# Performance work log

Hardware: AMD Instinct MI355X
Metric: run time of the kernel (lower is better)

Reference implementation:

```python
import jax, jax.numpy as jnp
import numpy as np

# dataset / mesh constants (from ds_props)
NX_PATCH, NY_PATCH = 10, 6       # Nx_patch * Ny_patch == 60 (hardcoded N_patch)
PX = 16                          # patch_size == out_patch_size
NPX, NPY = NX_PATCH * PX, NY_PATCH * PX
N_NODES = NPX * NPY              # 15360
HID = 128


def make_edge_idx(n, m):
    """Bidirectional 4-neighbor grid edges; n rows, m cols; node idx = j*n + i."""
    jj, ii = np.meshgrid(np.arange(m), np.arange(n - 1), indexing='ij')
    a = (jj * n + ii).ravel()
    e_v = np.concatenate([np.stack([a, a + 1]), np.stack([a + 1, a])], axis=1)
    ii2, jj2 = np.meshgrid(np.arange(n), np.arange(m - 1), indexing='ij')
    b = (jj2 * n + ii2).ravel()
    e_h = np.concatenate([np.stack([b, b + n]), np.stack([b + n, b])], axis=1)
    return np.concatenate([e_v, e_h], axis=1).astype(np.int32)  # [2, E]


def setup_inputs() -> dict:
    key = jax.random.key(0)
    ks = jax.random.split(key, 6)
    bs, seq_len, in_dim = 4, 32, 1024
    s = 0.02
    return {
        'patch_vectors': jax.random.normal(ks[0], (bs, seq_len * 60, in_dim), jnp.float32),
        'W1': jax.random.normal(ks[1], (in_dim, 512), jnp.float32) * s,
        'b1': jnp.zeros((512,), jnp.float32),
        'W2': jax.random.normal(ks[2], (512, HID), jnp.float32) * s,
        'b2': jnp.zeros((HID,), jnp.float32),
        'Wg': jax.random.normal(ks[3], (HID + 4, 3), jnp.float32) * s,
        'bg': jnp.zeros((3,), jnp.float32),
        'edge_index': jnp.asarray(make_edge_idx(NPY, NPX)),  # make_edge_idx(Ny_mesh, Nx_mesh)
    }


def _coord_feats():
    # patch index per pixel: (Npx, Npy, 2), raw integer patch coords (as in source)
    xg, yg = jnp.meshgrid(jnp.arange(NX_PATCH), jnp.arange(NY_PATCH), indexing='ij')
    pidx = jnp.stack([xg, yg], axis=-1).astype(jnp.float32)          # (Nx_patch, Ny_patch, 2)
    pidx = jnp.repeat(jnp.repeat(pidx, PX, axis=0), PX, axis=1)       # (Npx, Npy, 2)
    # pixel index within patch, normalized by global max (px-1), tiled over patches
    xp, yp = jnp.meshgrid(jnp.arange(PX), jnp.arange(PX), indexing='ij')
    pix = jnp.stack([xp, yp], axis=-1).astype(jnp.float32) / (PX - 1)
    pix = jnp.tile(pix, (NX_PATCH, NY_PATCH, 1))                      # (Npx, Npy, 2)
    return pidx, pix


def reference(patch_vectors, W1, b1, W2, b2, Wg, bg, edge_index):
    bs, tot_patchs, _ = patch_vectors.shape
    seq_len = tot_patchs // 60
    # input MLP: Linear -> softplus -> Linear
    h = jax.nn.softplus(patch_vectors @ W1 + b1) @ W2 + b2            # (bs, tot, 128)
    h = h.reshape(bs, seq_len, NX_PATCH, NY_PATCH, HID)
    # patch_to_px: repeat_interleave upsample to pixel mesh
    h = jnp.repeat(jnp.repeat(h, PX, axis=2), PX, axis=3)             # (bs, seq, Npx, Npy, 128)
    pidx, pix = _coord_feats()
    pidx = jnp.broadcast_to(pidx, (bs, seq_len, NPX, NPY, 2))
    pix = jnp.broadcast_to(pix, (bs, seq_len, NPX, NPY, 2))
    feat = jnp.concatenate([h, pidx, pix], axis=-1)                   # (..., 132)
    feat = feat.reshape(bs * seq_len, N_NODES, HID + 4)               # (B, N, 132)
    # GCNConv with self-loops: D^{-1/2} (A+I) D^{-1/2} X W + b
    src, dst = edge_index[0], edge_index[1]
    deg = 1.0 + jax.ops.segment_sum(jnp.ones(src.shape, jnp.float32), dst, num_segments=N_NODES)
    dinv = jax.lax.rsqrt(deg)
    norm = dinv[src] * dinv[dst]                                      # (E,)
    xw = feat @ Wg                                                    # (B, N, 3)
    agg = jax.vmap(lambda m: jax.ops.segment_sum(m, dst, num_segments=N_NODES))(
        xw[:, src, :] * norm[None, :, None])                          # scatter-add over edges
    out = agg + xw * (1.0 / deg)[None, :, None] + bg                  # self-loop term + bias
    return out.reshape(-1, NPX, NPY, 3)
```

## Files before the change

kernel.cpp:

```cpp
#include <hip/hip_runtime.h>
#include <math.h>

typedef __bf16 bf16_t;
typedef __bf16 bf16x8 __attribute__((ext_vector_type(8)));
typedef float f32x4 __attribute__((ext_vector_type(4)));

#define M_ROWS 7680
#define N1 512
#define K1 1024
#define NPX 160
#define NPY 96
#define BDIM 128
#define NPATCH 60
#define NPIX (BDIM*NPX*NPY)

#define OFF_WGEFF   0
#define OFF_BIASEFF 1536
#define OFF_CF      2048
#define OFF_HWPART  71168
#define OFF_W1T     255488

#define BM 64
#define BN 64
#define BK 64
#define LDT 72

__global__ __launch_bounds__(256) void prep_kernel(
    const float* __restrict__ W1, const float* __restrict__ W2,
    const float* __restrict__ b2, const float* __restrict__ Wg,
    const float* __restrict__ bg, float* __restrict__ ws)
{
    const int t = threadIdx.x;
    if (blockIdx.x < 128) {
        __shared__ bf16_t tile[64][72];
        const int k0 = (blockIdx.x & 15) * 64;
        const int n0 = (blockIdx.x >> 4) * 64;
        bf16_t* W1T = (bf16_t*)(ws + OFF_W1T);
#pragma unroll
        for (int i = 0; i < 4; ++i) {
            int idx = t + i * 256;
            int r = idx >> 4, ch = idx & 15;
            float4 v = *(const float4*)(W1 + (size_t)(k0 + r) * N1 + n0 + ch * 4);
            bf16_t* dst = &tile[r][ch * 4];
            dst[0] = (bf16_t)v.x; dst[1] = (bf16_t)v.y;
            dst[2] = (bf16_t)v.z; dst[3] = (bf16_t)v.w;
        }
        __syncthreads();
#pragma unroll
        for (int i = 0; i < 2; ++i) {
            int idx = t + i * 256;
            int nr = idx >> 3, kc = idx & 7;
            bf16x8 o;
#pragma unroll
            for (int j = 0; j < 8; ++j) o[j] = tile[kc * 8 + j][nr];
            *(bf16x8*)(W1T + (size_t)(n0 + nr) * K1 + k0 + kc * 8) = o;
        }
    } else if (blockIdx.x == 128) {
#pragma unroll
        for (int rep = 0; rep < 2; ++rep) {
            int j = t + rep * 256;
            float a0 = 0.f, a1 = 0.f, a2 = 0.f;
            for (int k = 0; k < 128; ++k) {
                float w = W2[j * 128 + k];
                a0 = fmaf(w, Wg[k * 3 + 0], a0);
                a1 = fmaf(w, Wg[k * 3 + 1], a1);
                a2 = fmaf(w, Wg[k * 3 + 2], a2);
            }
            ws[OFF_WGEFF + j * 3 + 0] = a0;
            ws[OFF_WGEFF + j * 3 + 1] = a1;
            ws[OFF_WGEFF + j * 3 + 2] = a2;
        }
        if (t < 3) {
            float s = 0.f;
            for (int k = 0; k < 128; ++k) s = fmaf(b2[k], Wg[k * 3 + t], s);
            ws[OFF_BIASEFF + t] = s;
        }
    } else {
        int e = (blockIdx.x - 129) * 256 + t;
        int c = e % 3;
        int p = e / 3;
        int x = p / NPY, y = p % NPY;
        float wpx = Wg[128 * 3 + c], wpy = Wg[129 * 3 + c];
        float wqx = Wg[130 * 3 + c], wqy = Wg[131 * 3 + c];
        auto aff = [&](int xx, int yy) -> float {
            return (float)(xx >> 4) * wpx + (float)(yy >> 4) * wpy
                 + (float)(xx & 15) * (1.f / 15.f) * wqx
                 + (float)(yy & 15) * (1.f / 15.f) * wqy;
        };
        auto deg = [&](int xx, int yy) -> float {
            return 1.f + (xx > 0) + (xx < NPX - 1) + (yy > 0) + (yy < NPY - 1);
        };
        float degc = deg(x, y);
        float s = 0.f;
        if (x > 0)       s += rsqrtf(deg(x - 1, y)) * aff(x - 1, y);
        if (x < NPX - 1) s += rsqrtf(deg(x + 1, y)) * aff(x + 1, y);
        if (y > 0)       s += rsqrtf(deg(x, y - 1)) * aff(x, y - 1);
        if (y < NPY - 1) s += rsqrtf(deg(x, y + 1)) * aff(x, y + 1);
        ws[OFF_CF + e] = rsqrtf(degc) * s + aff(x, y) / degc + bg[c];
    }
}

static __device__ inline bf16x8 cvt8(float4 a, float4 b) {
    bf16x8 v;
    v[0] = (bf16_t)a.x; v[1] = (bf16_t)a.y; v[2] = (bf16_t)a.z; v[3] = (bf16_t)a.w;
    v[4] = (bf16_t)b.x; v[5] = (bf16_t)b.y; v[6] = (bf16_t)b.z; v[7] = (bf16_t)b.w;
    return v;
}

__global__ __launch_bounds__(512, 8) void gemm_mfma_kernel(
    const float* __restrict__ A,
    const float* __restrict__ b1,
    const float* __restrict__ ws,
    float* __restrict__ hw_part)
{
    __shared__ __align__(16) char smem[36864];
    bf16_t* sA = (bf16_t*)smem;
    bf16_t* sB = sA + 2 * BM * LDT;
    float* red = (float*)smem;
    const bf16_t* W1T = (const bf16_t*)(ws + OFF_W1T);

    const int bid = blockIdx.x;
    const int xcd = bid & 7;
    const int local = bid >> 3;
    const int nblk = local & 7;
    const int mblk = xcd * 15 + (local >> 3);
    const int m0 = mblk * BM;
    const int n0 = nblk * BN;

    const int t = threadIdx.x;
    const int lane = t & 63;
    const int wv = t >> 6;
    const int wr = wv & 1;
    const int wcn = wv >> 1;
    const int l15 = lane & 15, hi = lane >> 4;

    const int srow = t >> 3;
    const int oct = (t & 7) << 3;
    const float*  aptr = A   + (size_t)(m0 + srow) * K1 + oct;
    const bf16_t* bptr = W1T + (size_t)(n0 + srow) * K1 + oct;
    const int swoff = srow * LDT + oct;

    f32x4 acc[2];
    acc[0] = (f32x4)0.f; acc[1] = (f32x4)0.f;

    {
        float4 fa0 = *(const float4*)(aptr + 0);
        float4 fa1 = *(const float4*)(aptr + 4);
        uint4  ub0 = *(const uint4*)(bptr);
        *(bf16x8*)(sA + swoff) = cvt8(fa0, fa1);
        *(uint4*)(sB + swoff)  = ub0;
    }
    __syncthreads();

    int cur = 0;
    for (int ks = 0; ks < K1 / BK; ++ks) {
        float4 fa0, fa1; uint4 ub0;
        const bool pf = (ks < K1 / BK - 1);
        if (pf) {
            const float*  ap = aptr + (ks + 1) * BK;
            const bf16_t* bp = bptr + (ks + 1) * BK;
            fa0 = *(const float4*)(ap + 0);
            fa1 = *(const float4*)(ap + 4);
            ub0 = *(const uint4*)(bp);
        }
        const bf16_t* cA = sA + cur * (BM * LDT);
        const bf16_t* cB = sB + cur * (BM * LDT);
        bf16x8 af[2][2], bfr[2];
#pragma unroll
        for (int kk = 0; kk < 2; ++kk) {
#pragma unroll
            for (int mi = 0; mi < 2; ++mi)
                af[mi][kk] = *(const bf16x8*)(cA + (wr * 32 + mi * 16 + l15) * LDT + kk * 32 + hi * 8);
            bfr[kk] = *(const bf16x8*)(cB + (wcn * 16 + l15) * LDT + kk * 32 + hi * 8);
        }
#pragma unroll
        for (int kk = 0; kk < 2; ++kk)
#pragma unroll
            for (int mi = 0; mi < 2; ++mi)
                acc[mi] = __builtin_amdgcn_mfma_f32_16x16x32_bf16(
                    af[mi][kk], bfr[kk], acc[mi], 0, 0, 0);
        if (pf) {
            bf16_t* nA = sA + (cur ^ 1) * (BM * LDT);
            bf16_t* nB = sB + (cur ^ 1) * (BM * LDT);
            *(bf16x8*)(nA + swoff) = cvt8(fa0, fa1);
            *(uint4*)(nB + swoff)  = ub0;
        }
        __syncthreads();
        cur ^= 1;
    }

    const int n = n0 + wcn * 16 + l15;
    const float bb = b1[n];
    const float wg0 = ws[OFF_WGEFF + n * 3 + 0];
    const float wg1 = ws[OFF_WGEFF + n * 3 + 1];
    const float wg2 = ws[OFF_WGEFF + n * 3 + 2];
    const int jslot = (wcn & 1) * 16 + l15;

    float p[2][4][3];
#pragma unroll
    for (int mi = 0; mi < 2; ++mi)
#pragma unroll
        for (int r = 0; r < 4; ++r) {
            float z = acc[mi][r] + bb;
            float sp = fmaxf(z, 0.f) + __logf(1.f + __expf(-fabsf(z)));
            p[mi][r][0] = sp * wg0;
            p[mi][r][1] = sp * wg1;
            p[mi][r][2] = sp * wg2;
        }
    __syncthreads();
    if (wcn < 2) {
#pragma unroll
        for (int mi = 0; mi < 2; ++mi)
#pragma unroll
            for (int r = 0; r < 4; ++r) {
                int ml = wr * 32 + mi * 16 + hi * 4 + r;
                float* dst = red + (ml * 32 + jslot) * 3;
                dst[0] = p[mi][r][0]; dst[1] = p[mi][r][1]; dst[2] = p[mi][r][2];
            }
    }
    __syncthreads();
    if (wcn >= 2) {
#pragma unroll
        for (int mi = 0; mi < 2; ++mi)
#pragma unroll
            for (int r = 0; r < 4; ++r) {
                int ml = wr * 32 + mi * 16 + hi * 4 + r;
                float* dst = red + (ml * 32 + jslot) * 3;
                dst[0] += p[mi][r][0]; dst[1] += p[mi][r][1]; dst[2] += p[mi][r][2];
            }
    }
    __syncthreads();
    if (t < 192) {
        int m = t / 3, c = t - m * 3;
        float s = 0.f;
#pragma unroll
        for (int j = 0; j < 32; ++j) s += red[(m * 32 + j) * 3 + c];
        hw_part[((size_t)nblk * M_ROWS + m0 + m) * 3 + c] = s;
    }
}

__global__ __launch_bounds__(384) void stencil_kernel(
    const float* __restrict__ ws, float* __restrict__ out)
{
    __shared__ float hwl[3][6][3];
    const int blk = blockIdx.x;
    const int b = blk / 10;
    const int px0 = blk % 10;
    const int x0 = px0 * 16;
    const int t = threadIdx.x;

    if (t < 54) {
        int j = t / 3, c = t - (t / 3) * 3;
        int dxi = j / 6, py = j % 6;
        int px = px0 - 1 + dxi;
        float v = 0.f;
        if (px >= 0 && px < 10) {
            int m = b * NPATCH + px * 6 + py;
            v = ws[OFF_BIASEFF + c];
#pragma unroll
            for (int s = 0; s < 8; ++s)
                v += ws[OFF_HWPART + ((size_t)s * M_ROWS + m) * 3 + c];
        }
        hwl[dxi][py][c] = v;
    }
    __syncthreads();

    const int xr = t / 24;
    const int y0 = (t - xr * 24) * 4;
    const int x = x0 + xr;
    const float* cf = ws + OFF_CF;

    auto deg = [&](int xx, int yy) -> float {
        return 1.f + (xx > 0) + (xx < NPX - 1) + (yy > 0) + (yy < NPY - 1);
    };
    auto hwp = [&](int xx, int yy) -> const float* {
        return &hwl[(xx >> 4) - (px0 - 1)][yy >> 4][0];
    };

    float res[4][3];
#pragma unroll
    for (int i = 0; i < 4; ++i) {
        int y = y0 + i;
        float degc = deg(x, y);
        float dinvc = rsqrtf(degc);
        float s0 = 0.f, s1 = 0.f, s2 = 0.f;
        auto tap = [&](int xx, int yy) {
            float dn = rsqrtf(deg(xx, yy));
            const float* h = hwp(xx, yy);
            s0 = fmaf(dn, h[0], s0);
            s1 = fmaf(dn, h[1], s1);
            s2 = fmaf(dn, h[2], s2);
        };
        if (x > 0)       tap(x - 1, y);
        if (x < NPX - 1) tap(x + 1, y);
        if (y > 0)       tap(x, y - 1);
        if (y < NPY - 1) tap(x, y + 1);
        const float* hs = hwp(x, y);
        const float* c = cf + (x * NPY + y) * 3;
        float inv_deg = 1.f / degc;
        res[i][0] = c[0] + fmaf(dinvc, s0, hs[0] * inv_deg);
        res[i][1] = c[1] + fmaf(dinvc, s1, hs[1] * inv_deg);
        res[i][2] = c[2] + fmaf(dinvc, s2, hs[2] * inv_deg);
    }
    float4 v0 = {res[0][0], res[0][1], res[0][2], res[1][0]};
    float4 v1 = {res[1][1], res[1][2], res[2][0], res[2][1]};
    float4 v2 = {res[2][2], res[3][0], res[3][1], res[3][2]};
    size_t p0 = ((size_t)b * NPX + x) * NPY + y0;
    float* o = out + p0 * 3;
    *(float4*)(o + 0) = v0;
    *(float4*)(o + 4) = v1;
    *(float4*)(o + 8) = v2;
}

extern "C" void kernel_launch(void* const* d_in, const int* in_sizes, int n_in,
                              void* d_out, int out_size, void* d_ws, size_t ws_size,
                              hipStream_t stream) {
    const float* pv = (const float*)d_in[0];
    const float* W1 = (const float*)d_in[1];
    const float* b1 = (const float*)d_in[2];
    const float* W2 = (const float*)d_in[3];
    const float* b2 = (const float*)d_in[4];
    const float* Wg = (const float*)d_in[5];
    const float* bg = (const float*)d_in[6];

    float* ws = (float*)d_ws;
    float* out = (float*)d_out;

    hipLaunchKernelGGL(prep_kernel, dim3(309), dim3(256), 0, stream,
                       W1, W2, b2, Wg, bg, ws);
    hipLaunchKernelGGL(gemm_mfma_kernel, dim3(960), dim3(512), 0, stream,
                       pv, b1, ws, ws + OFF_HWPART);
    hipLaunchKernelGGL(stencil_kernel, dim3(1280), dim3(384), 0, stream,
                       ws, out);
}
```

Measured before the change: 55.17 us.

## Pre-convert activations to bf16 and stream GEMM tiles via global_load_lds

When the workspace is large enough, the prep kernel gains 960 extra blocks that convert the fp32 activation matrix to bf16 in workspace. A new 256-thread GEMM kernel then loads swizzled bf16 A and W1T tiles directly into LDS with global_load_lds, double-buffered, so the fp32 loads and in-register conversion leave the GEMM loop. The cost is an extra full write and re-read of a 15 MB bf16 copy of A plus an added dependency between prep and GEMM. If the workspace is too small, the old path is kept.

```diff
diff --git a/kernel.cpp b/kernel.cpp
--- a/kernel.cpp
+++ b/kernel.cpp
@@ -4,6 +4,7 @@
 typedef __bf16 bf16_t;
 typedef __bf16 bf16x8 __attribute__((ext_vector_type(8)));
 typedef float f32x4 __attribute__((ext_vector_type(4)));
+typedef unsigned int u32;
 
 #define M_ROWS 7680
 #define N1 512
@@ -19,16 +20,32 @@
 #define OFF_CF      2048
 #define OFF_HWPART  71168
 #define OFF_W1T     255488
+#define OFF_ABF     517632
+#define WS_NEED_BYTES ((size_t)OFF_ABF * 4 + (size_t)M_ROWS * K1 * 2)
 
 #define BM 64
 #define BN 64
 #define BK 64
 #define LDT 72
 
+static __device__ __forceinline__ void gll16(const void* g, void* l) {
+    __builtin_amdgcn_global_load_lds(
+        (const __attribute__((address_space(1))) u32*)g,
+        (__attribute__((address_space(3))) u32*)l, 16, 0, 0);
+}
+
+static __device__ inline bf16x8 cvt8(float4 a, float4 b) {
+    bf16x8 v;
+    v[0] = (bf16_t)a.x; v[1] = (bf16_t)a.y; v[2] = (bf16_t)a.z; v[3] = (bf16_t)a.w;
+    v[4] = (bf16_t)b.x; v[5] = (bf16_t)b.y; v[6] = (bf16_t)b.z; v[7] = (bf16_t)b.w;
+    return v;
+}
+
 __global__ __launch_bounds__(256) void prep_kernel(
-    const float* __restrict__ W1, const float* __restrict__ W2,
-    const float* __restrict__ b2, const float* __restrict__ Wg,
-    const float* __restrict__ bg, float* __restrict__ ws)
+    const float* __restrict__ A, const float* __restrict__ W1,
+    const float* __restrict__ W2, const float* __restrict__ b2,
+    const float* __restrict__ Wg, const float* __restrict__ bg,
+    float* __restrict__ ws)
 {
     const int t = threadIdx.x;
     if (blockIdx.x < 128) {
@@ -75,7 +92,7 @@
             for (int k = 0; k < 128; ++k) s = fmaf(b2[k], Wg[k * 3 + t], s);
             ws[OFF_BIASEFF + t] = s;
         }
-    } else {
+    } else if (blockIdx.x < 309) {
         int e = (blockIdx.x - 129) * 256 + t;
         int c = e % 3;
         int p = e / 3;
@@ -97,21 +114,151 @@
         if (y > 0)       s += rsqrtf(deg(x, y - 1)) * aff(x, y - 1);
         if (y < NPY - 1) s += rsqrtf(deg(x, y + 1)) * aff(x, y + 1);
         ws[OFF_CF + e] = rsqrtf(degc) * s + aff(x, y) / degc + bg[c];
-    }
-}
-
-static __device__ inline bf16x8 cvt8(float4 a, float4 b) {
-    bf16x8 v;
-    v[0] = (bf16_t)a.x; v[1] = (bf16_t)a.y; v[2] = (bf16_t)a.z; v[3] = (bf16_t)a.w;
-    v[4] = (bf16_t)b.x; v[5] = (bf16_t)b.y; v[6] = (bf16_t)b.z; v[7] = (bf16_t)b.w;
-    return v;
-}
-
-__global__ __launch_bounds__(512, 8) void gemm_mfma_kernel(
-    const float* __restrict__ A,
+    } else {
+        bf16_t* Abf = (bf16_t*)(ws + OFF_ABF);
+        const int m0 = (blockIdx.x - 309) * 8;
+#pragma unroll
+        for (int j = 0; j < 4; ++j) {
+            int c = t + j * 256;
+            int row = c >> 7;
+            int col8 = c & 127;
+            const float* src = A + (size_t)(m0 + row) * K1 + col8 * 8;
+            float4 v0 = *(const float4*)(src);
+            float4 v1 = *(const float4*)(src + 4);
+            *(bf16x8*)(Abf + (size_t)(m0 + row) * K1 + col8 * 8) = cvt8(v0, v1);
+        }
+    }
+}
+
+__global__ __launch_bounds__(256) void gemm_gll_kernel(
     const float* __restrict__ b1,
     const float* __restrict__ ws,
     float* __restrict__ hw_part)
+{
+    __shared__ __align__(16) char smem[32768];
+    bf16_t* sA = (bf16_t*)smem;
+    bf16_t* sB = sA + 2 * 64 * 64;
+    float* red = (float*)smem;
+    const bf16_t* W1T = (const bf16_t*)(ws + OFF_W1T);
+    const bf16_t* Abf = (const bf16_t*)(ws + OFF_ABF);
+
+    const int bid = blockIdx.x;
+    const int xcd = bid & 7;
+    const int local = bid >> 3;
+    const int nblk = local & 7;
+    const int mblk = xcd * 15 + (local >> 3);
+    const int m0 = mblk * BM;
+    const int n0 = nblk * BN;
+
+    const int t = threadIdx.x;
+    const int lane = t & 63;
+    const int wv = t >> 6;
+    const int wr = wv >> 1, wc = wv & 1;
+    const int l15 = lane & 15, hi = lane >> 4;
+    const int x7 = l15 & 7;
+
+    const int rbase0 = 8 * (2 * wv + 0) + (lane >> 3);
+    const int c16src = (lane & 7) ^ (lane >> 3);
+    const bf16_t* aSrc0 = Abf + (size_t)(m0 + rbase0) * K1 + c16src * 8;
+    const bf16_t* aSrc1 = aSrc0 + (size_t)8 * K1;
+    const bf16_t* bSrc0 = W1T + (size_t)(n0 + rbase0) * K1 + c16src * 8;
+    const bf16_t* bSrc1 = bSrc0 + (size_t)8 * K1;
+    const int ldsOffA0 = (2 * wv + 0) * 512;
+    const int ldsOffA1 = (2 * wv + 1) * 512;
+
+    int aoff[2][2], boff[2][2];
+#pragma unroll
+    for (int mi = 0; mi < 2; ++mi)
+#pragma unroll
+        for (int kk = 0; kk < 2; ++kk) {
+            aoff[mi][kk] = (wr * 32 + mi * 16 + l15) * 64 + ((kk * 4 + hi) ^ x7) * 8;
+            boff[mi][kk] = (wc * 32 + mi * 16 + l15) * 64 + ((kk * 4 + hi) ^ x7) * 8;
+        }
+
+    f32x4 acc[2][2];
+#pragma unroll
+    for (int i = 0; i < 2; ++i)
+#pragma unroll
+        for (int j = 0; j < 2; ++j) acc[i][j] = (f32x4)0.f;
+
+    gll16(aSrc0, sA + ldsOffA0);
+    gll16(aSrc1, sA + ldsOffA1);
+    gll16(bSrc0, sB + ldsOffA0);
+    gll16(bSrc1, sB + ldsOffA1);
+    __syncthreads();
+
+    int cur = 0;
+    for (int ks = 0; ks < K1 / BK; ++ks) {
+        if (ks < K1 / BK - 1) {
+            const int koff = (ks + 1) * BK;
+            const int nb = (cur ^ 1) * 4096;
+            gll16(aSrc0 + koff, sA + nb + ldsOffA0);
+            gll16(aSrc1 + koff, sA + nb + ldsOffA1);
+            gll16(bSrc0 + koff, sB + nb + ldsOffA0);
+            gll16(bSrc1 + koff, sB + nb + ldsOffA1);
+        }
+        const bf16_t* cA = sA + cur * 4096;
+        const bf16_t* cB = sB + cur * 4096;
+        bf16x8 af[2][2], bfr[2][2];
+#pragma unroll
+        for (int i = 0; i < 2; ++i)
+#pragma unroll
+            for (int kk = 0; kk < 2; ++kk) {
+                af[i][kk]  = *(const bf16x8*)(cA + aoff[i][kk]);
+                bfr[i][kk] = *(const bf16x8*)(cB + boff[i][kk]);
+            }
+#pragma unroll
+        for (int kk = 0; kk < 2; ++kk)
+#pragma unroll
+            for (int mi = 0; mi < 2; ++mi)
+#pragma unroll
+                for (int ni = 0; ni < 2; ++ni)
+                    acc[mi][ni] = __builtin_amdgcn_mfma_f32_16x16x32_bf16(
+                        af[mi][kk], bfr[ni][kk], acc[mi][ni], 0, 0, 0);
+        __syncthreads();
+        cur ^= 1;
+    }
+
+    float b1v[2], wgv[2][3];
+#pragma unroll
+    for (int ni = 0; ni < 2; ++ni) {
+        int n = n0 + wc * 32 + ni * 16 + l15;
+        b1v[ni]    = b1[n];
+        wgv[ni][0] = ws[OFF_WGEFF + n * 3 + 0];
+        wgv[ni][1] = ws[OFF_WGEFF + n * 3 + 1];
+        wgv[ni][2] = ws[OFF_WGEFF + n * 3 + 2];
+    }
+#pragma unroll
+    for (int mi = 0; mi < 2; ++mi)
+#pragma unroll
+        for (int r = 0; r < 4; ++r) {
+            float p0 = 0.f, p1 = 0.f, p2 = 0.f;
+#pragma unroll
+            for (int ni = 0; ni < 2; ++ni) {
+                float z = acc[mi][ni][r] + b1v[ni];
+                float sp = fmaxf(z, 0.f) + __logf(1.f + __expf(-fabsf(z)));
+                p0 = fmaf(sp, wgv[ni][0], p0);
+                p1 = fmaf(sp, wgv[ni][1], p1);
+                p2 = fmaf(sp, wgv[ni][2], p2);
+            }
+            int ml = wr * 32 + mi * 16 + hi * 4 + r;
+            int j  = wc * 16 + l15;
+            float* dst = red + (ml * 32 + j) * 3;
+            dst[0] = p0; dst[1] = p1; dst[2] = p2;
+        }
+    __syncthreads();
+    if (t < 192) {
+        int m = t / 3, c = t - m * 3;
+        float s = 0.f;
+#pragma unroll
+        for (int j = 0; j < 32; ++j) s += red[(m * 32 + j) * 3 + c];
+        hw_part[((size_t)nblk * M_ROWS + m0 + m) * 3 + c] = s;
+    }
+}
+
+__global__ __launch_bounds__(512, 8) void gemm_mfma_kernel(
+    const float* __restrict__ A, const float* __restrict__ b1,
+    const float* __restrict__ ws, float* __restrict__ hw_part)
 {
     __shared__ __align__(16) char smem[36864];
     bf16_t* sA = (bf16_t*)smem;
@@ -325,11 +472,19 @@
 
     float* ws = (float*)d_ws;
     float* out = (float*)d_out;
-
-    hipLaunchKernelGGL(prep_kernel, dim3(309), dim3(256), 0, stream,
-                       W1, W2, b2, Wg, bg, ws);
-    hipLaunchKernelGGL(gemm_mfma_kernel, dim3(960), dim3(512), 0, stream,
-                       pv, b1, ws, ws + OFF_HWPART);
+    const bool big = ws_size >= WS_NEED_BYTES;
+
+    if (big) {
+        hipLaunchKernelGGL(prep_kernel, dim3(309 + 960), dim3(256), 0, stream,
+                           pv, W1, W2, b2, Wg, bg, ws);
+        hipLaunchKernelGGL(gemm_gll_kernel, dim3(960), dim3(256), 0, stream,
+                           b1, ws, ws + OFF_HWPART);
+    } else {
+        hipLaunchKernelGGL(prep_kernel, dim3(309), dim3(256), 0, stream,
+                           pv, W1, W2, b2, Wg, bg, ws);
+        hipLaunchKernelGGL(gemm_mfma_kernel, dim3(960), dim3(512), 0, stream,
+                           pv, b1, ws, ws + OFF_HWPART);
+    }
     hipLaunchKernelGGL(stencil_kernel, dim3(1280), dim3(384), 0, stream,
                        ws, out);
 }
```

New measurement: 51.98 us, median of 2. -5.8%, faster.
